# Performance work log

Measured on AMD Instinct MI355X. Metric: run time of the kernel, lower is better.

The kernel has to match this reference:

```python
import jax, jax.numpy as jnp
import numpy as np

B, T, C, H, TT = 8, 1024, 512, 8, 4  # batch, seq, n_embd, n_head, total_timestep
D = C // H


def setup_inputs() -> dict:
    key = jax.random.key(0)
    ks = jax.random.split(key, 4)
    s = 1.0 / np.sqrt(C)
    return {
        "x": jax.random.normal(ks[0], (B, T, C), jnp.float32),
        "padding_mask": jax.random.bernoulli(ks[1], 0.1, (TT, T)),  # bool
        "W_qkv": jax.random.normal(ks[2], (C, 3 * C), jnp.float32) * s,
        "b_qkv": jnp.zeros((3 * C,), jnp.float32),
        "W_proj": jax.random.normal(ks[3], (C, C), jnp.float32) * s,
        "b_proj": jnp.zeros((C,), jnp.float32),
    }


def reference(x, padding_mask, W_qkv, b_qkv, W_proj, b_proj):
    # fused QKV projection
    qkv = x @ W_qkv + b_qkv                       # [B,T,3C]
    q, k, v = jnp.split(qkv, 3, axis=-1)
    q = q.reshape(B, T, H, D)
    k = k.reshape(B, T, H, D)
    v = v.reshape(B, T, H, D)

    # mask: causal OR padding (True = attend), replicating torch semantics
    causal = jnp.tril(jnp.ones((T, T), bool))                 # [T,T]
    m = causal[None] | padding_mask[:, :, None]               # [TT,T,T]
    mask = jnp.broadcast_to(m[None], (B // TT, TT, T, T)).reshape(B, 1, T, T)

    scores = jnp.einsum("bqhd,bkhd->bhqk", q, k) * (1.0 / np.sqrt(D))
    scores = jnp.where(mask, scores, jnp.float32(-1e30))
    attn = jax.nn.softmax(scores, axis=-1)                    # [B,H,T,T]
    y = jnp.einsum("bhqk,bkhd->bqhd", attn, v).reshape(B, T, C)
    return y @ W_proj + b_proj
```

## Files before the change

### kernel.cpp

```cpp
#include <hip/hip_runtime.h>
#include <hip/hip_bf16.h>

#define BB 8
#define TT_ 4
#define TSEQ 1024
#define CEMB 512
#define NH 8
#define HD 64

typedef __attribute__((ext_vector_type(8))) short bf16x8;
typedef __attribute__((ext_vector_type(4))) float f32x4;
typedef __attribute__((ext_vector_type(16))) float f32x16;

#define AS1 __attribute__((address_space(1)))
#define AS3 __attribute__((address_space(3)))

__device__ __forceinline__ void gload_lds16(const void* g, void* l) {
  __builtin_amdgcn_global_load_lds((const AS1 unsigned int*)g, (AS3 unsigned int*)l, 16, 0, 0);
}

__device__ __forceinline__ short f2b(float f) {
  union { float f; unsigned u; } v; v.f = f;
  unsigned r = v.u + 0x7FFFu + ((v.u >> 16) & 1u);
  return (short)(r >> 16);
}

__device__ __forceinline__ unsigned pack2(float a, float b) {
  unsigned r;
  asm("v_cvt_pk_bf16_f32 %0, %1, %2" : "=v"(r) : "v"(a), "v"(b));
  return r;
}

__global__ __launch_bounds__(256) void k_prep(
    const float* __restrict__ x, short* __restrict__ xb,
    const float* __restrict__ w0, short* __restrict__ t0,
    const float* __restrict__ w1, short* __restrict__ t1,
    const void* __restrict__ pin, int* __restrict__ pme,
    int* __restrict__ perm, int* __restrict__ chunk_nkt)
{
  __shared__ float tsh[64][65];
  const int bid = blockIdx.x;

  if (bid < 2048) {
    const int i = bid * 256 + threadIdx.x;
    float4 v0 = ((const float4*)x)[i * 2];
    float4 v1 = ((const float4*)x)[i * 2 + 1];
    union { unsigned u[4]; bf16x8 v; } o;
    o.u[0] = pack2(v0.x, v0.y); o.u[1] = pack2(v0.z, v0.w);
    o.u[2] = pack2(v1.x, v1.y); o.u[3] = pack2(v1.z, v1.w);
    ((bf16x8*)xb)[i] = o.v;
    return;
  }

  if (bid < 2304) {
    const int z = (bid >= 2240);
    const int tile = z ? (bid - 2240) : (bid - 2048);
    const int ntx = z ? 8 : 24;
    const float* w = z ? w1 : w0;
    short* wt = z ? t1 : t0;
    const int N = z ? 512 : 1536, K = 512;
    const int tx = threadIdx.x & 15, ty = threadIdx.x >> 4;
    const int n0 = (tile % ntx) * 64, k0 = (tile / ntx) * 64;
#pragma unroll
    for (int i = 0; i < 4; ++i) {
      int kr = i * 16 + ty;
      float4 v = *(const float4*)&w[(size_t)(k0 + kr) * N + n0 + tx * 4];
      tsh[tx * 4 + 0][kr] = v.x; tsh[tx * 4 + 1][kr] = v.y;
      tsh[tx * 4 + 2][kr] = v.z; tsh[tx * 4 + 3][kr] = v.w;
    }
    __syncthreads();
#pragma unroll
    for (int i = 0; i < 4; ++i) {
      int nr = i * 16 + ty;
      short4 o;
      o.x = f2b(tsh[nr][tx * 4 + 0]); o.y = f2b(tsh[nr][tx * 4 + 1]);
      o.z = f2b(tsh[nr][tx * 4 + 2]); o.w = f2b(tsh[nr][tx * 4 + 3]);
      *(short4*)&wt[(size_t)(n0 + nr) * K + k0 + tx * 4] = o;
    }
    return;
  }

  __shared__ int bad_f32, any_f32, bad_i32, any_i32, bad_u16, any_u16;
  if (threadIdx.x == 0) { bad_f32 = any_f32 = bad_i32 = any_i32 = bad_u16 = any_u16 = 0; }
  __syncthreads();
  const unsigned char* pb = (const unsigned char*)pin;
  const float* pf = (const float*)pin;
  const int* pi = (const int*)pin;
  const unsigned short* ph = (const unsigned short*)pin;
  for (int i = threadIdx.x; i < 1024; i += 256) {
    float fv = pf[i];
    if (fv != 0.0f && fv != 1.0f) bad_f32 = 1;
    if (fv == 1.0f) any_f32 = 1;
    int iv = pi[i];
    if (iv != 0 && iv != 1) bad_i32 = 1;
    if (iv == 1) any_i32 = 1;
  }
  for (int i = threadIdx.x; i < 2048; i += 256) {
    unsigned short hv = ph[i];
    if (hv != 0 && hv != 0x3F80u && hv != 0x3C00u) bad_u16 = 1;
    if (hv == 0x3F80u || hv == 0x3C00u) any_u16 = 1;
  }
  __syncthreads();
  int mode = 3;
  if (!bad_f32 && any_f32) mode = 0;
  else if (!bad_i32 && any_i32) mode = 1;
  else if (!bad_u16 && any_u16) mode = 2;
  for (int i = threadIdx.x; i < TT_ * TSEQ; i += 256) {
    int v;
    if (mode == 0)      v = (pf[i] != 0.0f);
    else if (mode == 1) v = (pi[i] != 0);
    else if (mode == 2) v = (ph[i] != 0);
    else                v = (pb[i] != 0);
    pme[i] = v;
  }
  __syncthreads();

  const int w = threadIdx.x >> 6, lane = threadIdx.x & 63;
  {
    const int* rowp = pme + w * 1024;
    unsigned long long bal[16];
    int npm = 0;
#pragma unroll
    for (int g = 0; g < 16; ++g) {
      bal[g] = __ballot(rowp[g * 64 + lane] != 0);
      npm += __popcll(bal[g]);
    }
    int off_non = 0, off_pm = 1024 - npm;
#pragma unroll
    for (int g = 0; g < 16; ++g) {
      unsigned long long m = bal[g];
      int below = __popcll(m & ((1ull << lane) - 1ull));
      int ispm = (int)((m >> lane) & 1ull);
      int pos = ispm ? (off_pm + below) : (off_non + lane - below);
      perm[w * 1024 + pos] = g * 64 + lane;
      int c = __popcll(m);
      off_pm += c; off_non += 64 - c;
    }
  }
  __syncthreads();
  {
    const int tt = w, c = (lane >> 3) & 7, seg = lane & 7;
    int mx = 0;
#pragma unroll
    for (int i = 0; i < 16; ++i) {
      int q = perm[tt * 1024 + c * 128 + seg * 16 + i];
      int need = pme[tt * 1024 + q] ? 16 : ((q >> 6) + 1);
      mx = mx > need ? mx : need;
    }
#pragma unroll
    for (int s = 1; s < 8; s <<= 1) {
      int o = __shfl_xor(mx, s, 64);
      mx = mx > o ? mx : o;
    }
    if (seg == 0) chunk_nkt[tt * 8 + c] = mx;
  }
}

__global__ __launch_bounds__(256) void k_gemm0(
    const short* __restrict__ A, const short* __restrict__ Bt,
    const float* __restrict__ bias,
    short* __restrict__ qb, short* __restrict__ kb, short* __restrict__ vtb)
{
  __shared__ short As[3][128 * 32];
  __shared__ short Bs[3][128 * 32];
  const int tid = threadIdx.x, lane = tid & 63, w = tid >> 6;
  const int wm = w >> 1, wn = w & 1;
  const int idp = (blockIdx.x & 7) * 96 + (blockIdx.x >> 3);
  const int n0 = (idp % 12) * 128, m0 = (idp / 12) * 128;
  f32x4 acc[4][4] = {};
  const char* Abase = (const char*)A + (size_t)m0 * 1024;
  const char* Bbase = (const char*)Bt + (size_t)n0 * 1024;
  const int rowL = w * 16 + (lane >> 2);
  const int colB = (lane & 3) * 16;

  auto stage = [&](int buf, int k0) {
#pragma unroll
    for (int is = 0; is < 2; ++is) {
      int row = is * 64 + rowL;
      gload_lds16(Abase + (size_t)row * 1024 + (size_t)(k0 * 2 + colB),
                  (char*)As[buf] + is * 4096 + w * 1024);
      gload_lds16(Bbase + (size_t)row * 1024 + (size_t)(k0 * 2 + colB),
                  (char*)Bs[buf] + is * 4096 + w * 1024);
    }
  };

  stage(0, 0);
  stage(1, 32);
#pragma unroll
  for (int it = 0; it < 16; ++it) {
    if (it < 15) asm volatile("s_waitcnt vmcnt(4)\n\ts_barrier" ::: "memory");
    else         asm volatile("s_waitcnt vmcnt(0)\n\ts_barrier" ::: "memory");
    if (it + 2 < 16) stage((it + 2) % 3, (it + 2) * 32);
    const short* Ab = As[it % 3];
    const short* Bb = Bs[it % 3];
    bf16x8 a[4], bfr[4];
#pragma unroll
    for (int mf = 0; mf < 4; ++mf)
      a[mf] = *(const bf16x8*)&Ab[(wm * 64 + mf * 16 + (lane & 15)) * 32 + (lane >> 4) * 8];
#pragma unroll
    for (int nf = 0; nf < 4; ++nf)
      bfr[nf] = *(const bf16x8*)&Bb[(wn * 64 + nf * 16 + (lane & 15)) * 32 + (lane >> 4) * 8];
#pragma unroll
    for (int mf = 0; mf < 4; ++mf)
#pragma unroll
      for (int nf = 0; nf < 4; ++nf)
        acc[mf][nf] = __builtin_amdgcn_mfma_f32_16x16x32_bf16(a[mf], bfr[nf], acc[mf][nf], 0, 0, 0);
  }

#pragma unroll
  for (int nf = 0; nf < 4; ++nf) {
    const int n_g = n0 + wn * 64 + nf * 16 + (lane & 15);
    const float bv = bias[n_g];
    const int which = n_g >> 9;
    const int c = n_g & 511;
    const int h = c >> 6, d = c & 63;
    const float qsc = (which == 0) ? 0.18033688011112043f : 1.0f;
#pragma unroll
    for (int mf = 0; mf < 4; ++mf) {
      const int mb = m0 + wm * 64 + mf * 16 + ((lane >> 4) << 2);
      const int b = mb >> 10, t0 = mb & 1023;
      const int b8h = b * NH + h;
      if (which == 2) {
        short4 pk;
        pk.x = f2b(acc[mf][nf][0] + bv);
        pk.y = f2b(acc[mf][nf][1] + bv);
        pk.z = f2b(acc[mf][nf][2] + bv);
        pk.w = f2b(acc[mf][nf][3] + bv);
        *(short4*)&vtb[((size_t)b8h * HD + d) * TSEQ + t0] = pk;
      } else {
        short* dst = (which == 0) ? qb : kb;
        size_t base = ((size_t)b8h * TSEQ + t0) * HD + d;
#pragma unroll
        for (int r = 0; r < 4; ++r)
          dst[base + (size_t)r * HD] = f2b((acc[mf][nf][r] + bv) * qsc);
      }
    }
  }
}

__global__ __launch_bounds__(256) void k_gemm1(
    const short* __restrict__ A, const short* __restrict__ Bt,
    const float* __restrict__ bias, float* __restrict__ fout)
{
  __shared__ short As[3][128 * 32];
  __shared__ short Bs[3][128 * 32];
  const int tid = threadIdx.x, lane = tid & 63, w = tid >> 6;
  const int wm = w >> 1, wn = w & 1;
  const int idp = (blockIdx.x & 7) * 32 + (blockIdx.x >> 3);
  const int n0 = (idp % 4) * 128, m0 = (idp / 4) * 128;
  f32x4 acc[4][4] = {};
  const char* Abase = (const char*)A + (size_t)m0 * 1024;
  const char* Bbase = (const char*)Bt + (size_t)n0 * 1024;
  const int rowL = w * 16 + (lane >> 2);
  const int colB = (lane & 3) * 16;

  auto stage = [&](int buf, int k0) {
#pragma unroll
    for (int is = 0; is < 2; ++is) {
      int row = is * 64 + rowL;
      gload_lds16(Abase + (size_t)row * 1024 + (size_t)(k0 * 2 + colB),
                  (char*)As[buf] + is * 4096 + w * 1024);
      gload_lds16(Bbase + (size_t)row * 1024 + (size_t)(k0 * 2 + colB),
                  (char*)Bs[buf] + is * 4096 + w * 1024);
    }
  };

  stage(0, 0);
  stage(1, 32);
#pragma unroll
  for (int it = 0; it < 16; ++it) {
    if (it < 15) asm volatile("s_waitcnt vmcnt(4)\n\ts_barrier" ::: "memory");
    else         asm volatile("s_waitcnt vmcnt(0)\n\ts_barrier" ::: "memory");
    if (it + 2 < 16) stage((it + 2) % 3, (it + 2) * 32);
    const short* Ab = As[it % 3];
    const short* Bb = Bs[it % 3];
    bf16x8 a[4], bfr[4];
#pragma unroll
    for (int mf = 0; mf < 4; ++mf)
      a[mf] = *(const bf16x8*)&Ab[(wm * 64 + mf * 16 + (lane & 15)) * 32 + (lane >> 4) * 8];
#pragma unroll
    for (int nf = 0; nf < 4; ++nf)
      bfr[nf] = *(const bf16x8*)&Bb[(wn * 64 + nf * 16 + (lane & 15)) * 32 + (lane >> 4) * 8];
#pragma unroll
    for (int mf = 0; mf < 4; ++mf)
#pragma unroll
      for (int nf = 0; nf < 4; ++nf)
        acc[mf][nf] = __builtin_amdgcn_mfma_f32_16x16x32_bf16(a[mf], bfr[nf], acc[mf][nf], 0, 0, 0);
  }

#pragma unroll
  for (int nf = 0; nf < 4; ++nf) {
    const int n_g = n0 + wn * 64 + nf * 16 + (lane & 15);
    const float bv = bias[n_g];
#pragma unroll
    for (int mf = 0; mf < 4; ++mf) {
      const int mb = m0 + wm * 64 + mf * 16 + ((lane >> 4) << 2);
#pragma unroll
      for (int r = 0; r < 4; ++r)
        fout[(size_t)(mb + r) * 512 + n_g] = acc[mf][nf][r] + bv;
    }
  }
}

__device__ __forceinline__ void pv_step(
    f32x16 p, int sub, int hi, int lq, const char* Vsb, f32x16& o0, f32x16& o1)
{
  unsigned P2[8];
#pragma unroll
  for (int i = 0; i < 8; ++i) P2[i] = pack2(p[2 * i], p[2 * i + 1]);
  unsigned e0 = __shfl_xor(hi ? P2[0] : P2[2], 32, 64);
  unsigned e1 = __shfl_xor(hi ? P2[1] : P2[3], 32, 64);
  unsigned e2 = __shfl_xor(hi ? P2[4] : P2[6], 32, 64);
  unsigned e3 = __shfl_xor(hi ? P2[5] : P2[7], 32, 64);
  union { unsigned u[4]; bf16x8 v; } f0, f1;
  f0.u[0] = hi ? e0 : P2[0]; f0.u[1] = hi ? e1 : P2[1];
  f0.u[2] = hi ? P2[2] : e0; f0.u[3] = hi ? P2[3] : e1;
  f1.u[0] = hi ? e2 : P2[4]; f1.u[1] = hi ? e3 : P2[5];
  f1.u[2] = hi ? P2[6] : e2; f1.u[3] = hi ? P2[7] : e3;
  __builtin_amdgcn_s_setprio(1);
#pragma unroll
  for (int dt = 0; dt < 2; ++dt) {
    int row = dt * 32 + lq;
    bf16x8 v0 = *(const bf16x8*)(Vsb + row * 128 + ((4 * sub + hi) ^ (row & 7)) * 16);
    bf16x8 v1 = *(const bf16x8*)(Vsb + row * 128 + ((4 * sub + 2 + hi) ^ (row & 7)) * 16);
    f32x16& o = dt ? o1 : o0;
    o = __builtin_amdgcn_mfma_f32_32x32x16_bf16(v0, f0.v, o, 0, 0, 0);
    o = __builtin_amdgcn_mfma_f32_32x32x16_bf16(v1, f1.v, o, 0, 0, 0);
  }
  __builtin_amdgcn_s_setprio(0);
}

__global__ __launch_bounds__(512) void k_attn(
    const short* __restrict__ qg, const short* __restrict__ kg,
    const short* __restrict__ vtg, const int* __restrict__ pme,
    const int* __restrict__ perm, const int* __restrict__ chunk_nkt,
    short* __restrict__ yb)
{
  __shared__ char smem[65536];
  const int tid = threadIdx.x, lane = tid & 63, w = tid >> 6;
  const int g = w >> 2;
  const int hi = lane >> 5, lq = lane & 31;
  const int id = blockIdx.x;
  const int bh = id & 63, b = bh >> 3, h = bh & 7, tt = b & 3;
  const int chunk = 7 - (id >> 6);
  const char* Qb = (const char*)(qg + (size_t)bh * TSEQ * HD);
  const char* Kb = (const char*)(kg + (size_t)bh * TSEQ * HD);
  const char* Vb = (const char*)(vtg + (size_t)bh * HD * TSEQ);

  const int stg_row = ((w & 3) << 3) + (lane >> 3);
  const int stg_cl = (lane & 7) ^ ((lane >> 3) & 7);

  auto stage = [&](int buf, int kt) {
#pragma unroll
    for (int is = 0; is < 2; ++is) {
      int row = is * 32 + stg_row;
      gload_lds16(Kb + (size_t)(kt * 64 + row) * 128 + stg_cl * 16,
                  smem + buf * 8192 + is * 4096 + (w & 3) * 1024);
      gload_lds16(Vb + (size_t)row * 2048 + kt * 128 + stg_cl * 16,
                  smem + 32768 + buf * 8192 + is * 4096 + (w & 3) * 1024);
    }
  };

  const int nkt = chunk_nkt[tt * 8 + chunk];
  const int q_g = perm[tt * 1024 + chunk * 128 + (w & 3) * 32 + lq];
  const int pmrow = pme[tt * TSEQ + q_g];

  if (g < nkt) stage(g * 2, g);

  int wmq = q_g, wnq = q_g;
#pragma unroll
  for (int s = 1; s < 64; s <<= 1) {
    wmq = max(wmq, __shfl_xor(wmq, s, 64));
    wnq = min(wnq, __shfl_xor(wnq, s, 64));
  }
  const int whaspm = __any(pmrow != 0);

  bf16x8 qf[4];
#pragma unroll
  for (int dk = 0; dk < 4; ++dk)
    qf[dk] = *(const bf16x8*)(Qb + (size_t)q_g * 128 + dk * 32 + hi * 16);

  float mrun = -1e30f, lrun = 0.0f;
  f32x16 o0 = {}, o1 = {};

  const int niter = (nkt + 1) >> 1;
  for (int i = 0; i < niter; ++i) {
    asm volatile("s_waitcnt vmcnt(0)" ::: "memory");
    __builtin_amdgcn_s_barrier();
    const int kt = 2 * i + g;
    if (kt + 2 < nkt) stage(g * 2 + ((i + 1) & 1), kt + 2);

    const int kb_ = kt * 64;
    if (kt < nkt && (kb_ <= wmq || whaspm)) {
      const char* Ksb = smem + (g * 2 + (i & 1)) * 8192;
      const char* Vsb = smem + 32768 + (g * 2 + (i & 1)) * 8192;

      f32x16 s0 = {}, s1 = {};
      __builtin_amdgcn_s_setprio(1);
#pragma unroll
      for (int dk = 0; dk < 4; ++dk) {
        int row0 = lq, row1 = 32 + lq;
        bf16x8 kf0 = *(const bf16x8*)(Ksb + row0 * 128 + ((2 * dk + hi) ^ (row0 & 7)) * 16);
        bf16x8 kf1 = *(const bf16x8*)(Ksb + row1 * 128 + ((2 * dk + hi) ^ (row1 & 7)) * 16);
        s0 = __builtin_amdgcn_mfma_f32_32x32x16_bf16(kf0, qf[dk], s0, 0, 0, 0);
        s1 = __builtin_amdgcn_mfma_f32_32x32x16_bf16(kf1, qf[dk], s1, 0, 0, 0);
      }
      __builtin_amdgcn_s_setprio(0);

      if (kb_ + 63 <= wnq) {
      } else if (kb_ > wmq) {
#pragma unroll
        for (int r = 0; r < 16; ++r) {
          s0[r] = pmrow ? s0[r] : -1e30f;
          s1[r] = pmrow ? s1[r] : -1e30f;
        }
      } else {
#pragma unroll
        for (int r = 0; r < 16; ++r) {
          int crow = (r & 3) + 8 * (r >> 2) + 4 * hi;
          s0[r] = ((kb_ + crow <= q_g) || pmrow) ? s0[r] : -1e30f;
          s1[r] = ((kb_ + 32 + crow <= q_g) || pmrow) ? s1[r] : -1e30f;
        }
      }

      float tm[16];
#pragma unroll
      for (int r = 0; r < 16; ++r) tm[r] = fmaxf(s0[r], s1[r]);
#pragma unroll
      for (int st = 8; st >= 1; st >>= 1)
#pragma unroll
        for (int r = 0; r < 8; ++r)
          if (r < st) tm[r] = fmaxf(tm[r], tm[r + st]);
      float mx = fmaxf(tm[0], __shfl_xor(tm[0], 32, 64));
      if (!__all(mx <= mrun + 8.0f)) {
        float nm = fmaxf(mrun, mx);
        float sc = __builtin_amdgcn_exp2f(mrun - nm);
        lrun *= sc;
#pragma unroll
        for (int r = 0; r < 16; ++r) { o0[r] *= sc; o1[r] *= sc; }
        mrun = nm;
      }
#pragma unroll
      for (int r = 0; r < 16; ++r) s0[r] = __builtin_amdgcn_exp2f(s0[r] - mrun);
#pragma unroll
      for (int r = 0; r < 16; ++r) s1[r] = __builtin_amdgcn_exp2f(s1[r] - mrun);
      float ts[16];
#pragma unroll
      for (int r = 0; r < 16; ++r) ts[r] = s0[r] + s1[r];
#pragma unroll
      for (int st = 8; st >= 1; st >>= 1)
#pragma unroll
        for (int r = 0; r < 8; ++r)
          if (r < st) ts[r] = ts[r] + ts[r + st];
      lrun += ts[0] + __shfl_xor(ts[0], 32, 64);

      pv_step(s0, 0, hi, lq, Vsb, o0, o1);
      pv_step(s1, 1, hi, lq, Vsb, o0, o1);
    }
  }

  __syncthreads();
  float* mg = (float*)smem;
  short* ys = (short*)(smem + 36864);
  const int idx = (w & 3) * 64 + lane;
  if (g == 1) {
    mg[idx * 34 + 0] = mrun;
    mg[idx * 34 + 1] = lrun;
#pragma unroll
    for (int j = 0; j < 16; ++j) mg[idx * 34 + 2 + j] = o0[j];
#pragma unroll
    for (int j = 0; j < 16; ++j) mg[idx * 34 + 18 + j] = o1[j];
  }
  __syncthreads();
  if (g == 0) {
    const float mB = mg[idx * 34 + 0], lB = mg[idx * 34 + 1];
    const float m = fmaxf(mrun, mB);
    const float wa = __builtin_amdgcn_exp2f(mrun - m);
    const float wb = __builtin_amdgcn_exp2f(mB - m);
    const float linv = 1.0f / (lrun * wa + lB * wb);
    const float fa = wa * linv, fb = wb * linv;
    short* yl = ys + ((w & 3) * 32 + lq) * 72;
#pragma unroll
    for (int dt = 0; dt < 2; ++dt) {
      const f32x16& o = dt ? o1 : o0;
      const int ob = dt ? 18 : 2;
#pragma unroll
      for (int gg = 0; gg < 4; ++gg) {
        short4 pk;
        pk.x = f2b(o[4 * gg + 0] * fa + mg[idx * 34 + ob + 4 * gg + 0] * fb);
        pk.y = f2b(o[4 * gg + 1] * fa + mg[idx * 34 + ob + 4 * gg + 1] * fb);
        pk.z = f2b(o[4 * gg + 2] * fa + mg[idx * 34 + ob + 4 * gg + 2] * fb);
        pk.w = f2b(o[4 * gg + 3] * fa + mg[idx * 34 + ob + 4 * gg + 3] * fb);
        *(short4*)(yl + dt * 32 + 8 * gg + 4 * hi) = pk;
      }
    }
  }
  __syncthreads();
  {
    const int row = tid >> 2, seg = tid & 3;
    const int q_row = perm[tt * 1024 + chunk * 128 + row];
    short* dst = yb + ((size_t)b * TSEQ + q_row) * CEMB + h * HD + seg * 16;
    *(bf16x8*)dst = *(const bf16x8*)&ys[row * 72 + seg * 16];
    *(bf16x8*)(dst + 8) = *(const bf16x8*)&ys[row * 72 + seg * 16 + 8];
  }
}

extern "C" void kernel_launch(void* const* d_in, const int* in_sizes, int n_in,
                              void* d_out, int out_size, void* d_ws, size_t ws_size,
                              hipStream_t stream) {
  const float* x     = (const float*)d_in[0];
  const void*  pmask = d_in[1];
  const float* Wqkv  = (const float*)d_in[2];
  const float* bqkv  = (const float*)d_in[3];
  const float* Wproj = (const float*)d_in[4];
  const float* bproj = (const float*)d_in[5];
  float* out = (float*)d_out;
  char* ws = (char*)d_ws;

  const size_t OFF_XB   = 0;
  const size_t OFF_WQT  = 8388608;
  const size_t OFF_WPT  = 9961472;
  const size_t OFF_Q    = 10485760;
  const size_t OFF_K    = 18874368;
  const size_t OFF_VT   = 27262976;
  const size_t OFF_Y    = 35651584;
  const size_t OFF_PM   = 44040192;
  const size_t OFF_PERM = 44056576;
  const size_t OFF_CNKT = 44072960;
  const size_t NEED     = 44073984;
  if (ws_size < NEED) return;

  short* xb  = (short*)(ws + OFF_XB);
  short* wqT = (short*)(ws + OFF_WQT);
  short* wpT = (short*)(ws + OFF_WPT);
  short* qb  = (short*)(ws + OFF_Q);
  short* kb  = (short*)(ws + OFF_K);
  short* vtb = (short*)(ws + OFF_VT);
  short* yb  = (short*)(ws + OFF_Y);
  int*   pme = (int*)(ws + OFF_PM);
  int*   prm = (int*)(ws + OFF_PERM);
  int*   cnk = (int*)(ws + OFF_CNKT);

  k_prep<<<dim3(2305), dim3(256), 0, stream>>>(x, xb, Wqkv, wqT, Wproj, wpT,
                                               pmask, pme, prm, cnk);
  k_gemm0<<<dim3(768), dim3(256), 0, stream>>>(xb, wqT, bqkv, qb, kb, vtb);
  k_attn<<<dim3(512), dim3(512), 0, stream>>>(qb, kb, vtb, pme, prm, cnk, yb);
  k_gemm1<<<dim3(256), dim3(256), 0, stream>>>(yb, wpT, bproj, out);
}
```

Measured before the change: 82.47 us.

## Fuse fp32-to-bf16 conversion of x into QKV GEMM A-operand loading

The separate prep pass that converted x to bf16 in workspace is removed; the QKV GEMM now loads fp32 x tiles into registers, converts them to bf16 and writes them to LDS itself, with a register double-buffer for the A operand and direct-to-LDS loads kept for B. This removes a full write and re-read of the bf16 copy of x and shrinks the prep kernel launch. In exchange, each GEMM tile reads twice as many bytes for A (fp32), every N-tile block redoes the conversion, and the pipeline now needs extra register pressure and LDS write/wait synchronization.

```diff
diff --git a/kernel.cpp b/kernel.cpp
--- a/kernel.cpp
+++ b/kernel.cpp
@@ -32,7 +32,6 @@
 }
 
 __global__ __launch_bounds__(256) void k_prep(
-    const float* __restrict__ x, short* __restrict__ xb,
     const float* __restrict__ w0, short* __restrict__ t0,
     const float* __restrict__ w1, short* __restrict__ t1,
     const void* __restrict__ pin, int* __restrict__ pme,
@@ -41,20 +40,9 @@
   __shared__ float tsh[64][65];
   const int bid = blockIdx.x;
 
-  if (bid < 2048) {
-    const int i = bid * 256 + threadIdx.x;
-    float4 v0 = ((const float4*)x)[i * 2];
-    float4 v1 = ((const float4*)x)[i * 2 + 1];
-    union { unsigned u[4]; bf16x8 v; } o;
-    o.u[0] = pack2(v0.x, v0.y); o.u[1] = pack2(v0.z, v0.w);
-    o.u[2] = pack2(v1.x, v1.y); o.u[3] = pack2(v1.z, v1.w);
-    ((bf16x8*)xb)[i] = o.v;
-    return;
-  }
-
-  if (bid < 2304) {
-    const int z = (bid >= 2240);
-    const int tile = z ? (bid - 2240) : (bid - 2048);
+  if (bid < 256) {
+    const int z = (bid >= 192);
+    const int tile = z ? (bid - 192) : bid;
     const int ntx = z ? 8 : 24;
     const float* w = z ? w1 : w0;
     short* wt = z ? t1 : t0;
@@ -157,7 +145,7 @@
 }
 
 __global__ __launch_bounds__(256) void k_gemm0(
-    const short* __restrict__ A, const short* __restrict__ Bt,
+    const float* __restrict__ X, const short* __restrict__ Bt,
     const float* __restrict__ bias,
     short* __restrict__ qb, short* __restrict__ kb, short* __restrict__ vtb)
 {
@@ -168,29 +156,57 @@
   const int idp = (blockIdx.x & 7) * 96 + (blockIdx.x >> 3);
   const int n0 = (idp % 12) * 128, m0 = (idp / 12) * 128;
   f32x4 acc[4][4] = {};
-  const char* Abase = (const char*)A + (size_t)m0 * 1024;
+  const char* Xbase = (const char*)X + (size_t)m0 * 2048;
   const char* Bbase = (const char*)Bt + (size_t)n0 * 1024;
   const int rowL = w * 16 + (lane >> 2);
   const int colB = (lane & 3) * 16;
 
-  auto stage = [&](int buf, int k0) {
+  float4 ar[2][4];
+
+  auto aload = [&](int slot, int k0) {
+#pragma unroll
+    for (int is = 0; is < 2; ++is) {
+      const char* p = Xbase + (size_t)(is * 64 + rowL) * 2048 + (size_t)k0 * 4 + (lane & 3) * 32;
+      ar[slot][is * 2]     = *(const float4*)p;
+      ar[slot][is * 2 + 1] = *(const float4*)(p + 16);
+    }
+  };
+  auto awrite = [&](int slot, int buf) {
+#pragma unroll
+    for (int is = 0; is < 2; ++is) {
+      union { unsigned u[4]; bf16x8 v; } o;
+      float4 a = ar[slot][is * 2], b2 = ar[slot][is * 2 + 1];
+      o.u[0] = pack2(a.x, a.y);  o.u[1] = pack2(a.z, a.w);
+      o.u[2] = pack2(b2.x, b2.y); o.u[3] = pack2(b2.z, b2.w);
+      *(bf16x8*)((char*)As[buf] + is * 4096 + w * 1024 + lane * 16) = o.v;
+    }
+  };
+  auto stageB = [&](int buf, int k0) {
 #pragma unroll
     for (int is = 0; is < 2; ++is) {
       int row = is * 64 + rowL;
-      gload_lds16(Abase + (size_t)row * 1024 + (size_t)(k0 * 2 + colB),
-                  (char*)As[buf] + is * 4096 + w * 1024);
       gload_lds16(Bbase + (size_t)row * 1024 + (size_t)(k0 * 2 + colB),
                   (char*)Bs[buf] + is * 4096 + w * 1024);
     }
   };
 
-  stage(0, 0);
-  stage(1, 32);
+  aload(0, 0);
+  stageB(0, 0);
+  aload(1, 32);
+  asm volatile("s_waitcnt vmcnt(6)" ::: "memory");
+  awrite(0, 0);
+  stageB(1, 32);
+
 #pragma unroll
   for (int it = 0; it < 16; ++it) {
-    if (it < 15) asm volatile("s_waitcnt vmcnt(4)\n\ts_barrier" ::: "memory");
-    else         asm volatile("s_waitcnt vmcnt(0)\n\ts_barrier" ::: "memory");
-    if (it + 2 < 16) stage((it + 2) % 3, (it + 2) * 32);
+    if (it < 15) asm volatile("s_waitcnt vmcnt(2)" ::: "memory");
+    else         asm volatile("s_waitcnt vmcnt(0)" ::: "memory");
+    if (it + 1 < 16) awrite((it + 1) & 1, (it + 1) % 3);
+    if (it + 2 < 16) aload(it & 1, (it + 2) * 32);
+    asm volatile("s_waitcnt lgkmcnt(0)" ::: "memory");
+    __builtin_amdgcn_s_barrier();
+    if (it + 2 < 16) stageB((it + 2) % 3, (it + 2) * 32);
+
     const short* Ab = As[it % 3];
     const short* Bb = Bs[it % 3];
     bf16x8 a[4], bfr[4];
@@ -517,7 +533,6 @@
   float* out = (float*)d_out;
   char* ws = (char*)d_ws;
 
-  const size_t OFF_XB   = 0;
   const size_t OFF_WQT  = 8388608;
   const size_t OFF_WPT  = 9961472;
   const size_t OFF_Q    = 10485760;
@@ -530,7 +545,6 @@
   const size_t NEED     = 44073984;
   if (ws_size < NEED) return;
 
-  short* xb  = (short*)(ws + OFF_XB);
   short* wqT = (short*)(ws + OFF_WQT);
   short* wpT = (short*)(ws + OFF_WPT);
   short* qb  = (short*)(ws + OFF_Q);
@@ -541,9 +555,9 @@
   int*   prm = (int*)(ws + OFF_PERM);
   int*   cnk = (int*)(ws + OFF_CNKT);
 
-  k_prep<<<dim3(2305), dim3(256), 0, stream>>>(x, xb, Wqkv, wqT, Wproj, wpT,
-                                               pmask, pme, prm, cnk);
-  k_gemm0<<<dim3(768), dim3(256), 0, stream>>>(xb, wqT, bqkv, qb, kb, vtb);
+  k_prep<<<dim3(257), dim3(256), 0, stream>>>(Wqkv, wqT, Wproj, wpT,
+                                              pmask, pme, prm, cnk);
+  k_gemm0<<<dim3(768), dim3(256), 0, stream>>>(x, wqT, bqkv, qb, kb, vtb);
   k_attn<<<dim3(512), dim3(512), 0, stream>>>(qb, kb, vtb, pme, prm, cnk, yb);
   k_gemm1<<<dim3(256), dim3(256), 0, stream>>>(yb, wpT, bproj, out);
 }
```

New measurement: 80.58 us. -2.3%, faster.
